# Kernel tuning notes

Measured on AMD Instinct MI355X. Metric: run time of the kernel, lower is better.

The kernel has to match this reference:

```python
import jax, jax.numpy as jnp
import numpy as np

B, N, DIN, H, D = 16, 1024, 128, 4, 32  # batch, n_agents, input_dim, heads, head_dim
NEG = -9e15


def setup_inputs() -> dict:
    key = jax.random.key(0)
    k1, k2, k3, k4 = jax.random.split(key, 4)
    x = jax.random.normal(k1, (B, N, DIN), jnp.float32)
    adj = jax.random.randint(k2, (B, N, N), 0, 2, jnp.int32)
    # params (xavier-ish scale)
    W = jax.random.normal(k3, (DIN, H * D), jnp.float32) * np.float32(1.0 / np.sqrt(DIN))
    b = jnp.zeros((H * D,), jnp.float32)
    a = jax.random.normal(k4, (2 * D, 1), jnp.float32) * np.float32(0.1)
    return {"x": x, "adj": adj, "W": W, "b": b, "a": a}


def reference(x, adj, W, b, a):
    Bb, Nn, _ = x.shape
    h = (x @ W + b).reshape(Bb, Nn, H, D)              # [B,N,H,D]
    # GAT trick: concat([h_i,h_j]) @ a == h_i@a[:D] + h_j@a[D:]
    a_i, a_j = a[:D, 0], a[D:, 0]
    e_i = jnp.einsum('bnhd,d->bnh', h, a_i)
    e_j = jnp.einsum('bnhd,d->bnh', h, a_j)
    e = e_i[:, :, None, :] + e_j[:, None, :, :]        # [B,N,N,H]
    e = jnp.where(e > 0, e, 0.2 * e)                   # LeakyReLU(0.2)
    e = jnp.where(adj[..., None] > 0, e, NEG)          # adjacency mask
    attn = jax.nn.softmax(e, axis=2)                   # softmax over neighbors j
    out = jnp.einsum('bijh,bjhd->bihd', attn, h)       # per-head aggregation
    return out.reshape(Bb, Nn, H * D)                  # concat heads
```

## Files before the change

kernel.cpp:

```cpp
#include <hip/hip_runtime.h>
#include <hip/hip_bf16.h>

#define Bdim 16
#define Ndim 1024
#define Hh   4
#define HDc  128
#define L2E  1.4426950408889634f

typedef float  float4v  __attribute__((ext_vector_type(4)));
typedef int    int4v    __attribute__((ext_vector_type(4)));
typedef short  short8   __attribute__((ext_vector_type(8)));
typedef unsigned short ushort4v __attribute__((ext_vector_type(4)));
typedef unsigned int   uint2v   __attribute__((ext_vector_type(2)));
typedef _Float16 f16x2 __attribute__((ext_vector_type(2)));
typedef _Float16 half8 __attribute__((ext_vector_type(8)));

__device__ __forceinline__ unsigned short bf16_rne(float f) {
    unsigned u = __float_as_uint(f);
    u = u + 0x7FFFu + ((u >> 16) & 1u);
    return (unsigned short)(u >> 16);
}
__device__ __forceinline__ unsigned short f16u(float f) {
    _Float16 h = (_Float16)f;
    union { _Float16 h; unsigned short u; } c; c.h = h; return c.u;
}
__device__ __forceinline__ void gl_lds16(const void* g, void* l) {
    __builtin_amdgcn_global_load_lds(
        (const __attribute__((address_space(1))) unsigned int*)g,
        (__attribute__((address_space(3))) unsigned int*)l, 16, 0, 0);
}
__device__ __forceinline__ unsigned pmax_mask(unsigned EE, unsigned FF,
                                              unsigned Ej, unsigned Fj, unsigned m) {
    union { unsigned u; f16x2 h; } a, b, c, d, r;
    a.u = EE; b.u = Ej; c.u = FF; d.u = Fj;
    r.h = __builtin_elementwise_max(a.h * b.h, c.h * d.h);
    return r.u & m;
}

__global__ __launch_bounds__(256) void split_w_kernel(
    const float* __restrict__ W, const float* __restrict__ bias,
    const float* __restrict__ a,
    unsigned short* __restrict__ WTh, unsigned short* __restrict__ WTl,
    float* __restrict__ bias2)
{
    const int t = threadIdx.x, blk = blockIdx.x;
    if (blk < 16) {
        int r  = blk * 8 + (t >> 5);
        int k0 = (t & 31) * 4;
        #pragma unroll
        for (int j = 0; j < 4; ++j) {
            float f = W[(size_t)(k0 + j) * HDc + r];
            unsigned short hi = bf16_rne(f);
            WTh[r * 128 + k0 + j] = hi;
            WTl[r * 128 + k0 + j] = bf16_rne(f - __uint_as_float((unsigned)hi << 16));
        }
    } else {
        #pragma unroll
        for (int rep = 0; rep < 2; ++rep) {
            int task = t + rep * 256;
            int row = task >> 2, hh = task & 3;
            float si = 0.f, sj = 0.f;
            #pragma unroll
            for (int d4 = 0; d4 < 8; ++d4) {
                float4v wv = *(const float4v*)(W + (size_t)row * HDc + hh * 32 + d4 * 4);
                float4v av = *(const float4v*)(a + d4 * 4);
                float4v bv = *(const float4v*)(a + 32 + d4 * 4);
                #pragma unroll
                for (int kk = 0; kk < 4; ++kk) {
                    si = fmaf(wv[kk], av[kk], si);
                    sj = fmaf(wv[kk], bv[kk], sj);
                }
            }
            float vi = si * L2E, vj = sj * L2E;
            unsigned short hi = bf16_rne(vi);
            WTh[(128 + hh) * 128 + row] = hi;
            WTl[(128 + hh) * 128 + row] = bf16_rne(vi - __uint_as_float((unsigned)hi << 16));
            unsigned short hj = bf16_rne(vj);
            WTh[(132 + hh) * 128 + row] = hj;
            WTl[(132 + hh) * 128 + row] = bf16_rne(vj - __uint_as_float((unsigned)hj << 16));
        }
        #pragma unroll
        for (int rp = 0; rp < 4; ++rp) {
            int idx = t + rp * 256;
            WTh[136 * 128 + idx] = 0;
            WTl[136 * 128 + idx] = 0;
        }
        if (t < 128) {
            bias2[t] = bias[t];
        } else if (t < 136) {
            int z = t - 128;
            const float* av = (z < 4) ? a : a + 32;
            int hh = z & 3;
            float s = 0.f;
            for (int d = 0; d < 32; ++d) s = fmaf(bias[hh * 32 + d], av[d], s);
            bias2[128 + z] = s * L2E;
        } else if (t < 144) {
            bias2[t] = 0.f;
        }
    }
}

__global__ __launch_bounds__(256, 1) void proj_kernel(
    const float* __restrict__ x,
    const unsigned short* __restrict__ WTg_h, const unsigned short* __restrict__ WTg_l,
    const float* __restrict__ bias2,
    unsigned short* __restrict__ hT,
    unsigned short* __restrict__ eiE, unsigned short* __restrict__ eiF,
    unsigned short* __restrict__ ejE, unsigned short* __restrict__ ejF)
{
    __shared__ __align__(16) unsigned char smem[106496];
    char* xls  = (char*)smem;
    char* wtls = (char*)smem + 32768;

    const int t = threadIdx.x, lane = t & 63, w = t >> 6;
    const int l16 = lane & 15, q = lane >> 4;
    const int nb = blockIdx.x * 64;
    const int b = nb >> 10, nloc = nb & 1023;

    {
        const char* gx = (const char*)(x + (size_t)nb * 128);
        int rh = lane >> 5, m = lane & 31;
        #pragma unroll
        for (int d = 0; d < 8; ++d) {
            int r = w * 16 + d * 2 + rh;
            int mg = m ^ (r & 7);
            gl_lds16(gx + (size_t)r * 512 + mg * 16, xls + (size_t)w * 8192 + d * 1024);
        }
    }
    {
        int rh = lane >> 4, m = lane & 15;
        #pragma unroll
        for (int d = 0; d < 18; ++d) {
            int n = w * 18 + d;
            if (n < 36) {
                int r = n * 4 + rh;
                gl_lds16((const char*)WTg_h + (size_t)r * 256 + (m ^ (r & 15)) * 16,
                         wtls + (size_t)n * 1024);
            } else {
                int r = (n - 36) * 4 + rh;
                gl_lds16((const char*)WTg_l + (size_t)r * 256 + (m ^ (r & 15)) * 16,
                         wtls + (size_t)n * 1024);
            }
        }
    }
    __syncthreads();

    float4v C[9];
    #pragma unroll
    for (int nt = 0; nt < 9; ++nt) C[nt] = (float4v){0.f, 0.f, 0.f, 0.f};

    #pragma unroll
    for (int ks = 0; ks < 4; ++ks) {
        short8 Ah, Al;
        {
            int r = w * 16 + l16;
            int c0 = (ks * 8 + q * 2) ^ (l16 & 7);
            int c1 = (ks * 8 + q * 2 + 1) ^ (l16 & 7);
            float4v x0 = *(const float4v*)(xls + (size_t)r * 512 + c0 * 16);
            float4v x1 = *(const float4v*)(xls + (size_t)r * 512 + c1 * 16);
            #pragma unroll
            for (int e = 0; e < 8; ++e) {
                float f = (e < 4) ? x0[e] : x1[e - 4];
                unsigned short hi = bf16_rne(f);
                Ah[e] = (short)hi;
                Al[e] = (short)bf16_rne(f - __uint_as_float((unsigned)hi << 16));
            }
        }
        #pragma unroll
        for (int nt = 0; nt < 9; ++nt) {
            const char* wb = wtls + (size_t)(nt * 16 + l16) * 256 + ((ks * 4 + q) ^ l16) * 16;
            short8 Bh = *(const short8*)wb;
            short8 Bl = *(const short8*)(wb + 36864);
            C[nt] = __builtin_amdgcn_mfma_f32_16x16x32_bf16(Ah, Bh, C[nt], 0, 0, 0);
            C[nt] = __builtin_amdgcn_mfma_f32_16x16x32_bf16(Ah, Bl, C[nt], 0, 0, 0);
            C[nt] = __builtin_amdgcn_mfma_f32_16x16x32_bf16(Al, Bh, C[nt], 0, 0, 0);
        }
    }

    {
        int node = nloc + w * 16 + q * 4;
        #pragma unroll
        for (int nt = 0; nt < 8; ++nt) {
            int col = nt * 16 + l16;
            float bv = bias2[col];
            ushort4v h4;
            #pragma unroll
            for (int r = 0; r < 4; ++r) h4[r] = f16u(C[nt][r] + bv);
            *(ushort4v*)(hT + (size_t)(b * HDc + col) * Ndim + node) = h4;
        }
        float bv = bias2[128 + l16];
        if (l16 < 8) {
            int hh = l16 & 3;
            ushort4v Ev, Fv;
            #pragma unroll
            for (int r = 0; r < 4; ++r) {
                float v = C[8][r] + bv;
                Ev[r] = f16u(__builtin_amdgcn_exp2f(v));
                Fv[r] = f16u(__builtin_amdgcn_exp2f(0.2f * v));
            }
            size_t off = (size_t)(b * Hh + hh) * Ndim + node;
            if (l16 < 4) { *(ushort4v*)(eiE + off) = Ev; *(ushort4v*)(eiF + off) = Fv; }
            else         { *(ushort4v*)(ejE + off) = Ev; *(ushort4v*)(ejF + off) = Fv; }
        }
    }
}

__global__ __launch_bounds__(256, 4) void gat_kernel(
    const int* __restrict__ adj, const unsigned short* __restrict__ hT,
    const unsigned short* __restrict__ eiE, const unsigned short* __restrict__ eiF,
    const unsigned short* __restrict__ ejE, const unsigned short* __restrict__ ejF,
    float* __restrict__ out)
{
    __shared__ __align__(16) unsigned char smem[40960];
    unsigned int* pkl = (unsigned int*)smem;
    unsigned int* lut = (unsigned int*)(smem + 2048);
    char* ejl = (char*)smem + 4096;
    char* hts = (char*)smem + 8192;

    const int t = threadIdx.x, lane = t & 63, w = t >> 6;
    const int L = blockIdx.x;
    const int b = (L & 7) + 8 * ((L >> 3) & 1);
    const int ibase = (L >> 4) * 16;
    const int i = lane & 15, q = lane >> 4;

    {
        const int m = lane & 31, rh = lane >> 5;
        const int r0 = w * 4 + rh;
        const int r1 = w * 4 + 2 + rh;
        const int4v* s0 = (const int4v*)(adj + ((size_t)(b * Ndim + ibase + r0)) * Ndim + m * 32);
        const int4v* s1 = (const int4v*)(adj + ((size_t)(b * Ndim + ibase + r1)) * Ndim + m * 32);
        int4v va[8], vb[8];
        #pragma unroll
        for (int u = 0; u < 8; ++u) va[u] = __builtin_nontemporal_load(s0 + u);
        #pragma unroll
        for (int u = 0; u < 8; ++u) vb[u] = __builtin_nontemporal_load(s1 + u);
        unsigned wa = 0, wb_ = 0;
        #pragma unroll
        for (int u = 0; u < 8; ++u) {
            unsigned na  = (unsigned)(va[u][0] | (va[u][1] << 1) | (va[u][2] << 2) | (va[u][3] << 3));
            unsigned nb_ = (unsigned)(vb[u][0] | (vb[u][1] << 1) | (vb[u][2] << 2) | (vb[u][3] << 3));
            wa  |= na  << (4 * u);
            wb_ |= nb_ << (4 * u);
        }
        pkl[r0 * 32 + ((m + r0) & 31)] = wa;
        pkl[r1 * 32 + ((m + r1) & 31)] = wb_;
    }
    if (t < 16) {
        lut[t * 2]     = ((t & 1) ? 0xFFFFu : 0u) | ((t & 2) ? 0xFFFF0000u : 0u);
        lut[t * 2 + 1] = ((t & 4) ? 0xFFFFu : 0u) | ((t & 8) ? 0xFFFF0000u : 0u);
    }
    const size_t eidx = (size_t)(b * Hh + w) * Ndim + ibase + i;
    const unsigned Eu = eiE[eidx], Fu = eiF[eidx];
    const unsigned EE = Eu | (Eu << 16);
    const unsigned FF = Fu | (Fu << 16);
    __syncthreads();

    const char* ghh = (const char*)(hT + (size_t)(b * HDc + w * 32) * Ndim);
    const int drow = lane >> 4;
    const int p16  = lane & 15;
    const char* gE = (const char*)(ejE + (size_t)(b * Hh + w) * Ndim);
    const char* gF = (const char*)(ejF + (size_t)(b * Hh + w) * Ndim);
    const int l5 = lane & 31;
    const char* esrc = (l5 < 16) ? gE + l5 * 16 : gF + (l5 - 16) * 16;

    const char* hrow0 = hts + (w * 32 + i) * 256;
    const char* hrow1 = hrow0 + 16 * 256;
    const char* ejw   = ejl + w * 1024;
    const uint2v* lut2 = (const uint2v*)lut;

    half8 ONES;
    #pragma unroll
    for (int e = 0; e < 8; ++e) ONES[e] = (_Float16)1.0f;

    float4v C0 = {0.f, 0.f, 0.f, 0.f};
    float4v C1 = {0.f, 0.f, 0.f, 0.f};
    float4v C2 = {0.f, 0.f, 0.f, 0.f};

    for (int ch = 0; ch < 8; ++ch) {
        if (ch) __syncthreads();
        #pragma unroll
        for (int u = 0; u < 8; ++u) {
            int d = u * 4 + drow;
            int c = p16 ^ (d & 15);
            gl_lds16(ghh + (size_t)d * 2048 + ch * 256 + c * 16,
                     hts + (w * 32 + u * 4) * 256);
        }
        gl_lds16(esrc + ch * 256, ejl + w * 1024);
        __syncthreads();

        #pragma unroll
        for (int jtl = 0; jtl < 4; ++jtl) {
            const int jt = ch * 4 + jtl;
            const int sb = jtl * 4 + q;
            half8 Bh0 = *(const half8*)(hrow0 + ((sb ^ i) << 4));
            half8 Bh1 = *(const half8*)(hrow1 + ((sb ^ i) << 4));
            int4v Ejp = *(const int4v*)(ejw + (sb << 4));
            int4v Fjp = *(const int4v*)(ejw + 256 + (sb << 4));
            unsigned bits = (pkl[i * 32 + ((jt + i) & 31)] >> (q * 8)) & 0xffu;
            uint2v m0 = lut2[bits & 15];
            uint2v m1 = lut2[bits >> 4];

            union { unsigned u[4]; half8 v; } A;
            A.u[0] = pmax_mask(EE, FF, (unsigned)Ejp[0], (unsigned)Fjp[0], m0[0]);
            A.u[1] = pmax_mask(EE, FF, (unsigned)Ejp[1], (unsigned)Fjp[1], m0[1]);
            A.u[2] = pmax_mask(EE, FF, (unsigned)Ejp[2], (unsigned)Fjp[2], m1[0]);
            A.u[3] = pmax_mask(EE, FF, (unsigned)Ejp[3], (unsigned)Fjp[3], m1[1]);

            C0 = __builtin_amdgcn_mfma_f32_16x16x32_f16(A.v, Bh0, C0, 0, 0, 0);
            C1 = __builtin_amdgcn_mfma_f32_16x16x32_f16(A.v, Bh1, C1, 0, 0, 0);
            C2 = __builtin_amdgcn_mfma_f32_16x16x32_f16(A.v, ONES, C2, 0, 0, 0);
        }
    }

    float* outp = out + ((size_t)(b * Ndim + ibase)) * HDc + w * 32 + i;
    #pragma unroll
    for (int reg = 0; reg < 4; ++reg) {
        int row = q * 4 + reg;
        float rd = 1.0f / C2[reg];
        outp[(size_t)row * HDc]      = C0[reg] * rd;
        outp[(size_t)row * HDc + 16] = C1[reg] * rd;
    }
}

extern "C" void kernel_launch(void* const* d_in, const int* in_sizes, int n_in,
                              void* d_out, int out_size, void* d_ws, size_t ws_size,
                              hipStream_t stream) {
    const float* x    = (const float*)d_in[0];
    const int*   adj  = (const int*)d_in[1];
    const float* W    = (const float*)d_in[2];
    const float* bias = (const float*)d_in[3];
    const float* a    = (const float*)d_in[4];
    float* out = (float*)d_out;

    unsigned short* hT  = (unsigned short*)d_ws;
    unsigned short* eiE = hT  + (size_t)Bdim * HDc * Ndim;
    unsigned short* eiF = eiE + (size_t)Bdim * Hh * Ndim;
    unsigned short* ejE = eiF + (size_t)Bdim * Hh * Ndim;
    unsigned short* ejF = ejE + (size_t)Bdim * Hh * Ndim;
    unsigned short* WTh = ejF + (size_t)Bdim * Hh * Ndim;
    unsigned short* WTl = WTh + 144 * 128;
    float* bias2 = (float*)(WTl + 144 * 128);

    split_w_kernel<<<dim3(17), dim3(256), 0, stream>>>(W, bias, a, WTh, WTl, bias2);
    proj_kernel<<<dim3(256), dim3(256), 0, stream>>>(
        x, WTh, WTl, bias2, hT, eiE, eiF, ejE, ejF);
    gat_kernel<<<dim3(1024), dim3(256), 0, stream>>>(
        adj, hT, eiE, eiF, ejE, ejF, out);
}
```

Measured before the change: 156.6 us.

## Double GAT block row tile to 32 rows with 8 waves sharing h loads

Each gat_kernel block now handles 32 query rows with 512 threads (8 waves) instead of 16 rows with 4 waves. The two row-halves share the same staged h^T and e_j chunks in LDS, so each block issues half the per-row global loads of h. The LDS layout is reshuffled so e_j for all four heads fits in 2 KB and the LUT moves after it. The grid halves, which may reduce latency hiding per CU and lengthens barrier waits, since each barrier now covers 8 waves.

```diff
diff --git a/kernel.cpp b/kernel.cpp
--- a/kernel.cpp
+++ b/kernel.cpp
@@ -21,8 +21,7 @@
     return (unsigned short)(u >> 16);
 }
 __device__ __forceinline__ unsigned short f16u(float f) {
-    _Float16 h = (_Float16)f;
-    union { _Float16 h; unsigned short u; } c; c.h = h; return c.u;
+    union { _Float16 h; unsigned short u; } c; c.h = (_Float16)f; return c.u;
 }
 __device__ __forceinline__ void gl_lds16(const void* g, void* l) {
     __builtin_amdgcn_global_load_lds(
@@ -205,7 +204,7 @@
     }
 }
 
-__global__ __launch_bounds__(256, 4) void gat_kernel(
+__global__ __launch_bounds__(512, 4) void gat_kernel(
     const int* __restrict__ adj, const unsigned short* __restrict__ hT,
     const unsigned short* __restrict__ eiE, const unsigned short* __restrict__ eiF,
     const unsigned short* __restrict__ ejE, const unsigned short* __restrict__ ejF,
@@ -213,20 +212,21 @@
 {
     __shared__ __align__(16) unsigned char smem[40960];
     unsigned int* pkl = (unsigned int*)smem;
-    unsigned int* lut = (unsigned int*)(smem + 2048);
-    char* ejl = (char*)smem + 4096;
+    char* ejl = (char*)(smem + 4096);
+    unsigned int* lut = (unsigned int*)(smem + 6144);
     char* hts = (char*)smem + 8192;
 
-    const int t = threadIdx.x, lane = t & 63, w = t >> 6;
+    const int t = threadIdx.x, lane = t & 63, w8 = t >> 6;
+    const int hw = w8 & 3, ihalf = w8 >> 2;
     const int L = blockIdx.x;
     const int b = (L & 7) + 8 * ((L >> 3) & 1);
-    const int ibase = (L >> 4) * 16;
+    const int ibase = (L >> 4) * 32;
     const int i = lane & 15, q = lane >> 4;
 
     {
         const int m = lane & 31, rh = lane >> 5;
-        const int r0 = w * 4 + rh;
-        const int r1 = w * 4 + 2 + rh;
+        const int r0 = w8 * 4 + rh;
+        const int r1 = r0 + 2;
         const int4v* s0 = (const int4v*)(adj + ((size_t)(b * Ndim + ibase + r0)) * Ndim + m * 32);
         const int4v* s1 = (const int4v*)(adj + ((size_t)(b * Ndim + ibase + r1)) * Ndim + m * 32);
         int4v va[8], vb[8];
@@ -249,24 +249,26 @@
         lut[t * 2]     = ((t & 1) ? 0xFFFFu : 0u) | ((t & 2) ? 0xFFFF0000u : 0u);
         lut[t * 2 + 1] = ((t & 4) ? 0xFFFFu : 0u) | ((t & 8) ? 0xFFFF0000u : 0u);
     }
-    const size_t eidx = (size_t)(b * Hh + w) * Ndim + ibase + i;
+    const size_t eidx = (size_t)(b * Hh + hw) * Ndim + ibase + ihalf * 16 + i;
     const unsigned Eu = eiE[eidx], Fu = eiF[eidx];
     const unsigned EE = Eu | (Eu << 16);
     const unsigned FF = Fu | (Fu << 16);
     __syncthreads();
 
-    const char* ghh = (const char*)(hT + (size_t)(b * HDc + w * 32) * Ndim);
-    const int drow = lane >> 4;
-    const int p16  = lane & 15;
-    const char* gE = (const char*)(ejE + (size_t)(b * Hh + w) * Ndim);
-    const char* gF = (const char*)(ejF + (size_t)(b * Hh + w) * Ndim);
-    const int l5 = lane & 31;
-    const char* esrc = (l5 < 16) ? gE + l5 * 16 : gF + (l5 - 16) * 16;
-
-    const char* hrow0 = hts + (w * 32 + i) * 256;
+    const char* ghh = (const char*)(hT + (size_t)(b * HDc + hw * 32) * Ndim);
+    const int myrow = ihalf * 16 + i;
+    const char* hrow0 = hts + (hw * 32 + i) * 256;
     const char* hrow1 = hrow0 + 16 * 256;
-    const char* ejw   = ejl + w * 1024;
+    const char* ejw   = ejl + hw * 512;
     const uint2v* lut2 = (const uint2v*)lut;
+    const char* esrc;
+    {
+        int hsel = w8 * 2 + (lane >> 5);
+        int tab  = (lane >> 4) & 1;
+        const unsigned short* base = tab ? ejF : ejE;
+        esrc = (const char*)(base + (size_t)(b * Hh + hsel) * Ndim) + (lane & 15) * 16;
+    }
+    const int ddma = ihalf * 16 + (lane >> 4);
 
     half8 ONES;
     #pragma unroll
@@ -279,13 +281,13 @@
     for (int ch = 0; ch < 8; ++ch) {
         if (ch) __syncthreads();
         #pragma unroll
-        for (int u = 0; u < 8; ++u) {
-            int d = u * 4 + drow;
-            int c = p16 ^ (d & 15);
+        for (int u = 0; u < 4; ++u) {
+            int d = ddma + u * 4;
+            int c = (lane & 15) ^ (d & 15);
             gl_lds16(ghh + (size_t)d * 2048 + ch * 256 + c * 16,
-                     hts + (w * 32 + u * 4) * 256);
-        }
-        gl_lds16(esrc + ch * 256, ejl + w * 1024);
+                     hts + (hw * 32 + ihalf * 16 + u * 4) * 256);
+        }
+        if (w8 < 2) gl_lds16(esrc + ch * 256, ejl + w8 * 1024);
         __syncthreads();
 
         #pragma unroll
@@ -296,7 +298,7 @@
             half8 Bh1 = *(const half8*)(hrow1 + ((sb ^ i) << 4));
             int4v Ejp = *(const int4v*)(ejw + (sb << 4));
             int4v Fjp = *(const int4v*)(ejw + 256 + (sb << 4));
-            unsigned bits = (pkl[i * 32 + ((jt + i) & 31)] >> (q * 8)) & 0xffu;
+            unsigned bits = (pkl[myrow * 32 + ((jt + myrow) & 31)] >> (q * 8)) & 0xffu;
             uint2v m0 = lut2[bits & 15];
             uint2v m1 = lut2[bits >> 4];
 
@@ -312,7 +314,7 @@
         }
     }
 
-    float* outp = out + ((size_t)(b * Ndim + ibase)) * HDc + w * 32 + i;
+    float* outp = out + ((size_t)(b * Ndim + ibase + ihalf * 16)) * HDc + hw * 32 + i;
     #pragma unroll
     for (int reg = 0; reg < 4; ++reg) {
         int row = q * 4 + reg;
@@ -344,6 +346,6 @@
     split_w_kernel<<<dim3(17), dim3(256), 0, stream>>>(W, bias, a, WTh, WTl, bias2);
     proj_kernel<<<dim3(256), dim3(256), 0, stream>>>(
         x, WTh, WTl, bias2, hT, eiE, eiF, ejE, ejF);
-    gat_kernel<<<dim3(1024), dim3(256), 0, stream>>>(
+    gat_kernel<<<dim3(512), dim3(512), 0, stream>>>(
         adj, hT, eiE, eiF, ejE, ejF, out);
 }
```

After: 160.1 us. +2.2%, slower.
